# Performance work log

Hardware: AMD Instinct MI355X
Metric: run time of the kernel (lower is better)

## Reference

```python
import jax, jax.numpy as jnp
import numpy as np

B, N3, N4, DIM, HEADS, MLP = 256, 256, 64, 512, 8, 2048
EPS = 1e-5

def _sinusoid(n_position, d_hid):
    pos = np.arange(n_position)[:, None].astype(np.float64)
    i = np.arange(d_hid)[None, :]
    angle = pos / np.power(10000.0, 2 * (i // 2) / d_hid)
    tab = np.empty((n_position, d_hid))
    tab[:, 0::2] = np.sin(angle[:, 0::2])
    tab[:, 1::2] = np.cos(angle[:, 1::2])
    return jnp.asarray(tab[None], dtype=jnp.float32)  # [1, n, d]

def _ln(x, g, b):
    m = x.mean(-1, keepdims=True)
    v = ((x - m) ** 2).mean(-1, keepdims=True)
    return (x - m) / jnp.sqrt(v + EPS) * g + b

def setup_inputs() -> dict:
    key = jax.random.key(0)
    ks = jax.random.split(key, 12)
    s = 0.02
    d = {
        'f3': jax.random.normal(ks[0], (B, N3, DIM), jnp.float32),
        'f4': jax.random.normal(ks[1], (B, N4, DIM), jnp.float32),
        'pos3': _sinusoid(N3, DIM),
        'pos4': _sinusoid(N4, DIM),
        'ln1_g': jnp.ones((DIM,), jnp.float32), 'ln1_b': jnp.zeros((DIM,), jnp.float32),
        'ln2_g': jnp.ones((DIM,), jnp.float32), 'ln2_b': jnp.zeros((DIM,), jnp.float32),
        'ln3_g': jnp.ones((DIM,), jnp.float32), 'ln3_b': jnp.zeros((DIM,), jnp.float32),
        'Wq': jax.random.normal(ks[2], (DIM, DIM), jnp.float32) * s, 'bq': jnp.zeros((DIM,), jnp.float32),
        'Wk': jax.random.normal(ks[3], (DIM, DIM), jnp.float32) * s, 'bk': jnp.zeros((DIM,), jnp.float32),
        'Wv': jax.random.normal(ks[4], (DIM, DIM), jnp.float32) * s, 'bv': jnp.zeros((DIM,), jnp.float32),
        'Wr': jax.random.normal(ks[5], (DIM, DIM), jnp.float32) * s, 'br': jnp.zeros((DIM,), jnp.float32),
        'W1': jax.random.normal(ks[6], (DIM, MLP), jnp.float32) * s, 'b1': jnp.zeros((MLP,), jnp.float32),
        'W2': jax.random.normal(ks[7], (MLP, DIM), jnp.float32) * s, 'b2': jnp.zeros((DIM,), jnp.float32),
    }
    return d

def reference(f3, f4, pos3, pos4, ln1_g, ln1_b, ln2_g, ln2_b, ln3_g, ln3_b,
              Wq, bq, Wk, bk, Wv, bv, Wr, br, W1, b1, W2, b2):
    dk = DIM // HEADS
    f3n = _ln(f3, ln1_g, ln1_b)
    f4n = _ln(f4, ln2_g, ln2_b)
    # projections (dropout=0 -> eval mode)
    q = (f3n + pos3) @ Wq + bq  # [B,N3,D]
    k = (f4n + pos4) @ Wk + bk  # [B,N4,D]
    v = f4n @ Wv + bv           # [B,N4,D]
    # split heads along channel dim (contiguous slices == reshape with head major)
    q = q.reshape(B, N3, HEADS, dk).transpose(0, 2, 3, 1)  # [B,H,dk,N3]
    k = k.reshape(B, N4, HEADS, dk).transpose(0, 2, 3, 1)  # [B,H,dk,N4]
    v = v.reshape(B, N4, HEADS, dk).transpose(0, 2, 3, 1)  # [B,H,dv,N4]
    q = jax.nn.softmax(q, axis=2)  # softmax over head channels
    k = jax.nn.softmax(k, axis=3)  # softmax over key positions
    context = jnp.einsum('bhkn,bhvn->bhkv', k, v)          # [B,H,dk,dv]
    att = jnp.einsum('bhkv,bhkn->bhvn', context, q)        # [B,H,dv,N3]
    att = att.transpose(0, 3, 1, 2).reshape(B, N3, DIM)    # concat heads -> [B,N3,D]
    f3 = f3 + (att @ Wr + br)
    h = _ln(f3, ln3_g, ln3_b)
    h = jax.nn.gelu(h @ W1 + b1, approximate=False) @ W2 + b2
    return f3 + h
```

## Files before the change

### kernel.cpp

```cpp
#include <hip/hip_runtime.h>
#include <hip/hip_bf16.h>

typedef __attribute__((ext_vector_type(8))) short short8v;
typedef __attribute__((ext_vector_type(4))) float f32x4;
typedef __hip_bfloat16 bf16;

#define BDIM 512
#define NHEADS 8
#define DK 64
#define NBATCH 256
#define NN3 256
#define NN4 64
#define NMLP 2048

#define GLOAD_LDS16(g, l)                                                  \
  __builtin_amdgcn_global_load_lds(                                        \
      (const __attribute__((address_space(1))) void*)(g),                  \
      (__attribute__((address_space(3))) void*)(l), 16, 0, 0)

__device__ __forceinline__ float bf2f(short s) {
  union { short u[2]; float f; } cv;
  cv.u[0] = 0; cv.u[1] = s;
  return cv.f;
}
__device__ __forceinline__ short f2bf(float x) {
  bf16 h = __float2bfloat16(x);
  return *reinterpret_cast<short*>(&h);
}

__global__ __launch_bounds__(256) void convert_wt_kernel(
    const float* __restrict__ W, bf16* __restrict__ Wt, int K, int N) {
  int idx = blockIdx.x * 256 + threadIdx.x;
  if (idx >= K * N) return;
  int n = idx / K;
  int k = idx - n * K;
  Wt[idx] = __float2bfloat16(W[(size_t)k * N + n]);
}

__global__ __launch_bounds__(256) void ln_kernel(
    const float* __restrict__ x, const float* __restrict__ g,
    const float* __restrict__ beta, const float* __restrict__ pos, int nmod,
    bf16* __restrict__ out1, bf16* __restrict__ out2, bf16* __restrict__ raw) {
  int w = threadIdx.x >> 6, lane = threadIdx.x & 63;
  int row = blockIdx.x * 4 + w;
  int c0 = lane * 8;
  const float* xr = x + (size_t)row * BDIM + c0;
  float4 v0 = *(const float4*)xr;
  float4 v1 = *(const float4*)(xr + 4);
  float f[8] = {v0.x, v0.y, v0.z, v0.w, v1.x, v1.y, v1.z, v1.w};
  float s = 0.f, sq = 0.f;
#pragma unroll
  for (int i = 0; i < 8; i++) {
    s += f[i];
    sq += f[i] * f[i];
  }
#pragma unroll
  for (int o = 1; o <= 32; o <<= 1) {
    s += __shfl_xor(s, o);
    sq += __shfl_xor(sq, o);
  }
  float mean = s * (1.f / BDIM);
  float var = sq * (1.f / BDIM) - mean * mean;
  float rstd = rsqrtf(var + 1e-5f);
  float4 g0 = *(const float4*)(g + c0);
  float4 g1 = *(const float4*)(g + c0 + 4);
  float4 b0 = *(const float4*)(beta + c0);
  float4 b1 = *(const float4*)(beta + c0 + 4);
  float gg[8] = {g0.x, g0.y, g0.z, g0.w, g1.x, g1.y, g1.z, g1.w};
  float bb[8] = {b0.x, b0.y, b0.z, b0.w, b1.x, b1.y, b1.z, b1.w};
  float pv[8] = {};
  if (pos) {
    int n = row % nmod;
    const float* pr = pos + (size_t)n * BDIM + c0;
    float4 p0 = *(const float4*)pr;
    float4 p1 = *(const float4*)(pr + 4);
    pv[0] = p0.x; pv[1] = p0.y; pv[2] = p0.z; pv[3] = p0.w;
    pv[4] = p1.x; pv[5] = p1.y; pv[6] = p1.z; pv[7] = p1.w;
  }
  short8v o1, o2, rw;
#pragma unroll
  for (int i = 0; i < 8; i++) {
    float nv = (f[i] - mean) * rstd * gg[i] + bb[i];
    o1[i] = f2bf(nv + pv[i]);
    o2[i] = f2bf(nv);
    rw[i] = f2bf(f[i]);
  }
  size_t ob = (size_t)row * BDIM + c0;
  *(short8v*)(out1 + ob) = o1;
  if (out2) *(short8v*)(out2 + ob) = o2;
  if (raw) *(short8v*)(raw + ob) = rw;
}

__global__ __launch_bounds__(256) void lnb_kernel(
    const bf16* __restrict__ x, const float* __restrict__ g,
    const float* __restrict__ beta, bf16* __restrict__ out) {
  int w = threadIdx.x >> 6, lane = threadIdx.x & 63;
  int row = blockIdx.x * 4 + w;
  int c0 = lane * 8;
  short8v v = *(const short8v*)(x + (size_t)row * BDIM + c0);
  float f[8];
  float s = 0.f, sq = 0.f;
#pragma unroll
  for (int i = 0; i < 8; i++) {
    f[i] = bf2f(v[i]);
    s += f[i];
    sq += f[i] * f[i];
  }
#pragma unroll
  for (int o = 1; o <= 32; o <<= 1) {
    s += __shfl_xor(s, o);
    sq += __shfl_xor(sq, o);
  }
  float mean = s * (1.f / BDIM);
  float var = sq * (1.f / BDIM) - mean * mean;
  float rstd = rsqrtf(var + 1e-5f);
  float4 g0 = *(const float4*)(g + c0);
  float4 g1 = *(const float4*)(g + c0 + 4);
  float4 b0 = *(const float4*)(beta + c0);
  float4 b1 = *(const float4*)(beta + c0 + 4);
  float gg[8] = {g0.x, g0.y, g0.z, g0.w, g1.x, g1.y, g1.z, g1.w};
  float bb[8] = {b0.x, b0.y, b0.z, b0.w, b1.x, b1.y, b1.z, b1.w};
  short8v o1;
#pragma unroll
  for (int i = 0; i < 8; i++) o1[i] = f2bf((f[i] - mean) * rstd * gg[i] + bb[i]);
  *(short8v*)(out + (size_t)row * BDIM + c0) = o1;
}

template <int EPI>
__global__ __launch_bounds__(512) void gemm_kernel(
    const bf16* __restrict__ X, const bf16* __restrict__ Wt,
    const float* __restrict__ bias, const void* __restrict__ src, void* outp,
    int K, int ldx, int ldw, int N, int gridX) {
  extern __shared__ bf16 lds[];

  int nwg = gridDim.x;
  int cpx = nwg >> 3;
  int bid = blockIdx.x;
  int nb = (bid & 7) * cpx + (bid >> 3);
  int bx = nb % gridX, by = nb / gridX;
  int row0 = by * 128, col0 = bx * 128;

  int t = threadIdx.x, w = t >> 6, lane = t & 63;
  int wr = w >> 2, wc = w & 3;
  int r16 = lane & 15, kg = lane >> 4;
  int srow = lane >> 3;
  int scol = ((lane & 7) ^ srow) * 8;

  const bf16* gA0 = X + (size_t)(row0 + w * 16 + srow) * ldx + scol;
  const bf16* gB0 = Wt + (size_t)(col0 + w * 16 + srow) * ldw + scol;

  f32x4 acc[4][2] = {};

  auto stage = [&](int kt, int buf) {
    bf16* base = lds + buf * 16384;
    int ke = kt << 6;
#pragma unroll
    for (int j = 0; j < 2; j++) {
      GLOAD_LDS16(gA0 + ke + (size_t)j * 8 * ldx, base + (w * 16 + j * 8) * 64);
      GLOAD_LDS16(gB0 + ke + (size_t)j * 8 * ldw,
                  base + 8192 + (w * 16 + j * 8) * 64);
    }
  };

  auto compute = [&](int buf) {
    const char* base = (const char*)(lds + buf * 16384);
#pragma unroll
    for (int ksub = 0; ksub < 2; ksub++) {
      int cc = (ksub * 64 + kg * 16) ^ ((r16 & 7) << 4);
      short8v a[4], b[2];
#pragma unroll
      for (int m = 0; m < 4; m++)
        a[m] = *(const short8v*)(base + (wr * 64 + m * 16 + r16) * 128 + cc);
#pragma unroll
      for (int n = 0; n < 2; n++)
        b[n] = *(const short8v*)(base + 16384 + (wc * 32 + n * 16 + r16) * 128 + cc);
#pragma unroll
      for (int m = 0; m < 4; m++)
#pragma unroll
        for (int n = 0; n < 2; n++)
          acc[m][n] =
              __builtin_amdgcn_mfma_f32_16x16x32_bf16(a[m], b[n], acc[m][n], 0, 0, 0);
    }
  };

  int NT = K >> 6;
  stage(0, 0);
  stage(1, 1);
  for (int tt = 0; tt < NT; tt++) {
    if (tt < NT - 1)
      asm volatile("s_waitcnt vmcnt(4)" ::: "memory");
    else
      asm volatile("s_waitcnt vmcnt(0)" ::: "memory");
    __builtin_amdgcn_s_barrier();
    asm volatile("" ::: "memory");
    compute(tt & 1);
    asm volatile("" ::: "memory");
    __builtin_amdgcn_s_barrier();
    asm volatile("" ::: "memory");
    if (tt + 2 < NT) stage(tt + 2, tt & 1);
  }

#pragma unroll
  for (int n = 0; n < 2; n++) {
    int col = col0 + wc * 32 + n * 16 + r16;
    float bv = bias ? bias[col] : 0.f;
#pragma unroll
    for (int m = 0; m < 4; m++)
#pragma unroll
      for (int r = 0; r < 4; r++) {
        int row = row0 + wr * 64 + m * 16 + kg * 4 + r;
        size_t o = (size_t)row * N + col;
        float val = acc[m][n][r] + bv;
        if (EPI == 0) {
          ((bf16*)outp)[o] = __float2bfloat16(val);
        } else if (EPI == 1) {
          float gl = 0.5f * val * (1.f + erff(val * 0.70710678f));
          ((bf16*)outp)[o] = __float2bfloat16(gl);
        } else if (EPI == 3) {
          ((bf16*)outp)[o] = __float2bfloat16(bf2f(((const short*)src)[o]) + val);
        } else {
          ((float*)outp)[o] = bf2f(((const short*)src)[o]) + val;
        }
      }
  }
}

__global__ __launch_bounds__(256) void ctx_kernel(
    const bf16* __restrict__ kproj, const bf16* __restrict__ vbuf,
    bf16* __restrict__ ctxT) {
  int bh = blockIdx.x;
  int b = bh >> 3, h = bh & 7;
  __shared__ bf16 lk[NN4][DK], lv[NN4][DK];
  int t = threadIdx.x;
#pragma unroll
  for (int i = 0; i < 16; i++) {
    int idx = i * 256 + t;
    int n = idx >> 6, c = idx & 63;
    size_t gaddr = (size_t)b * NN4 * BDIM + (size_t)n * BDIM + h * DK + c;
    lk[n][c] = kproj[gaddr];
    lv[n][c] = vbuf[gaddr];
  }
  __syncthreads();
  if (t < 64) {
    int c = t;
    float e[NN4];
    float m = -1e30f;
#pragma unroll
    for (int n = 0; n < NN4; n++) {
      e[n] = bf2f(*(short*)&lk[n][c]);
      m = fmaxf(m, e[n]);
    }
    float s = 0.f;
#pragma unroll
    for (int n = 0; n < NN4; n++) {
      e[n] = __expf(e[n] - m);
      s += e[n];
    }
    float inv = 1.f / s;
#pragma unroll
    for (int n = 0; n < NN4; n++) lk[n][c] = __float2bfloat16(e[n] * inv);
  }
  __syncthreads();
  int vc = t >> 2;
  int kc0 = (t & 3) * 16;
  float acc[16] = {};
  for (int n = 0; n < NN4; n++) {
    float vv = __bfloat162float(lv[n][vc]);
#pragma unroll
    for (int i = 0; i < 16; i++)
      acc[i] += vv * __bfloat162float(lk[n][kc0 + i]);
  }
  size_t o = (size_t)bh * 4096 + (size_t)vc * 64 + kc0;
#pragma unroll
  for (int i = 0; i < 16; i++) ctxT[o + i] = __float2bfloat16(acc[i]);
}

__global__ __launch_bounds__(256) void att_kernel(
    const bf16* __restrict__ qproj, const bf16* __restrict__ ctxT,
    bf16* __restrict__ att) {
  int bh = blockIdx.x;
  int b = bh >> 3, h = bh & 7;
  int t = threadIdx.x, w = t >> 6, lane = t & 63;
  int r16 = lane & 15, kg = lane >> 4;
  f32x4 acc[4][4] = {};
  const bf16* qb = qproj + (size_t)b * NN3 * BDIM + h * DK;
  const bf16* cb = ctxT + (size_t)bh * 4096;
  short8v bb[2][4];
#pragma unroll
  for (int kt = 0; kt < 2; kt++)
#pragma unroll
    for (int ni = 0; ni < 4; ni++)
      bb[kt][ni] = *(const short8v*)(cb + (ni * 16 + r16) * 64 + kt * 32 + kg * 8);
#pragma unroll
  for (int mi = 0; mi < 4; mi++) {
    int rrow = w * 64 + mi * 16 + r16;
    short8v a0 = *(const short8v*)(qb + (size_t)rrow * BDIM + kg * 8);
    short8v a1 = *(const short8v*)(qb + (size_t)rrow * BDIM + 32 + kg * 8);
    float f[16];
#pragma unroll
    for (int i = 0; i < 8; i++) {
      f[i] = bf2f(a0[i]);
      f[8 + i] = bf2f(a1[i]);
    }
    float m = f[0];
#pragma unroll
    for (int i = 1; i < 16; i++) m = fmaxf(m, f[i]);
    m = fmaxf(m, __shfl_xor(m, 16));
    m = fmaxf(m, __shfl_xor(m, 32));
    float s = 0.f;
#pragma unroll
    for (int i = 0; i < 16; i++) {
      f[i] = __expf(f[i] - m);
      s += f[i];
    }
    s += __shfl_xor(s, 16);
    s += __shfl_xor(s, 32);
    float inv = 1.f / s;
    short8v A0, A1;
#pragma unroll
    for (int i = 0; i < 8; i++) {
      A0[i] = f2bf(f[i] * inv);
      A1[i] = f2bf(f[8 + i] * inv);
    }
#pragma unroll
    for (int ni = 0; ni < 4; ni++) {
      acc[mi][ni] = __builtin_amdgcn_mfma_f32_16x16x32_bf16(A0, bb[0][ni], acc[mi][ni], 0, 0, 0);
      acc[mi][ni] = __builtin_amdgcn_mfma_f32_16x16x32_bf16(A1, bb[1][ni], acc[mi][ni], 0, 0, 0);
    }
  }
#pragma unroll
  for (int mi = 0; mi < 4; mi++)
#pragma unroll
    for (int ni = 0; ni < 4; ni++)
#pragma unroll
      for (int r = 0; r < 4; r++) {
        int row = w * 64 + mi * 16 + kg * 4 + r;
        int col = ni * 16 + r16;
        att[(size_t)(b * NN3 + row) * BDIM + h * DK + col] =
            __float2bfloat16(acc[mi][ni][r]);
      }
}

extern "C" void kernel_launch(void* const* d_in, const int* in_sizes, int n_in,
                              void* d_out, int out_size, void* d_ws, size_t ws_size,
                              hipStream_t stream) {
  const float* f3 = (const float*)d_in[0];
  const float* f4 = (const float*)d_in[1];
  const float* pos3 = (const float*)d_in[2];
  const float* pos4 = (const float*)d_in[3];
  const float* ln1_g = (const float*)d_in[4];
  const float* ln1_b = (const float*)d_in[5];
  const float* ln2_g = (const float*)d_in[6];
  const float* ln2_b = (const float*)d_in[7];
  const float* ln3_g = (const float*)d_in[8];
  const float* ln3_b = (const float*)d_in[9];
  const float* Wq = (const float*)d_in[10];
  const float* bq = (const float*)d_in[11];
  const float* Wk = (const float*)d_in[12];
  const float* bk = (const float*)d_in[13];
  const float* Wv = (const float*)d_in[14];
  const float* bv = (const float*)d_in[15];
  const float* Wr = (const float*)d_in[16];
  const float* br = (const float*)d_in[17];
  const float* W1 = (const float*)d_in[18];
  const float* b1 = (const float*)d_in[19];
  const float* W2 = (const float*)d_in[20];
  const float* b2 = (const float*)d_in[21];
  float* out = (float*)d_out;

  const int M3 = NBATCH * NN3;
  const int M4 = NBATCH * NN4;
  const int MC = M3 / 2;

  char* ws = (char*)d_ws;
  size_t off = 0;
  auto alloc = [&](size_t bytes) {
    size_t r = off;
    off = (off + bytes + 255) & ~(size_t)255;
    return r;
  };
  size_t oWqt = alloc((size_t)BDIM * BDIM * 2);
  size_t oWkt = alloc((size_t)BDIM * BDIM * 2);
  size_t oWvt = alloc((size_t)BDIM * BDIM * 2);
  size_t oWrt = alloc((size_t)BDIM * BDIM * 2);
  size_t oW1t = alloc((size_t)BDIM * NMLP * 2);
  size_t oW2t = alloc((size_t)BDIM * NMLP * 2);
  size_t oXQ = alloc((size_t)M3 * BDIM * 2);
  size_t oXK = alloc((size_t)M4 * BDIM * 2);
  size_t oXV = alloc((size_t)M4 * BDIM * 2);
  size_t oQF = alloc((size_t)M3 * BDIM * 2);
  size_t oKF = alloc((size_t)M4 * BDIM * 2);
  size_t oVF = alloc((size_t)M4 * BDIM * 2);
  size_t oF3B = alloc((size_t)M3 * BDIM * 2);
  size_t oCT = alloc((size_t)NBATCH * NHEADS * DK * DK * 2);
  size_t oH1 = alloc((size_t)MC * NMLP * 2);
  (void)ws_size;

  bf16* Wqt = (bf16*)(ws + oWqt);
  bf16* Wkt = (bf16*)(ws + oWkt);
  bf16* Wvt = (bf16*)(ws + oWvt);
  bf16* Wrt = (bf16*)(ws + oWrt);
  bf16* W1t = (bf16*)(ws + oW1t);
  bf16* W2t = (bf16*)(ws + oW2t);
  bf16* XQ = (bf16*)(ws + oXQ);
  bf16* XK = (bf16*)(ws + oXK);
  bf16* XV = (bf16*)(ws + oXV);
  bf16* QF = (bf16*)(ws + oQF);
  bf16* KF = (bf16*)(ws + oKF);
  bf16* VF = (bf16*)(ws + oVF);
  bf16* F3B = (bf16*)(ws + oF3B);
  bf16* CT = (bf16*)(ws + oCT);
  bf16* H1 = (bf16*)(ws + oH1);
  bf16* ATT = XQ;
  bf16* F3O = QF;
  bf16* YN = XQ;

  hipFuncSetAttribute((const void*)gemm_kernel<0>,
                      hipFuncAttributeMaxDynamicSharedMemorySize, 65536);
  hipFuncSetAttribute((const void*)gemm_kernel<1>,
                      hipFuncAttributeMaxDynamicSharedMemorySize, 65536);
  hipFuncSetAttribute((const void*)gemm_kernel<3>,
                      hipFuncAttributeMaxDynamicSharedMemorySize, 65536);
  hipFuncSetAttribute((const void*)gemm_kernel<4>,
                      hipFuncAttributeMaxDynamicSharedMemorySize, 65536);

  convert_wt_kernel<<<(BDIM * BDIM + 255) / 256, 256, 0, stream>>>(Wq, Wqt, BDIM, BDIM);
  convert_wt_kernel<<<(BDIM * BDIM + 255) / 256, 256, 0, stream>>>(Wk, Wkt, BDIM, BDIM);
  convert_wt_kernel<<<(BDIM * BDIM + 255) / 256, 256, 0, stream>>>(Wv, Wvt, BDIM, BDIM);
  convert_wt_kernel<<<(BDIM * BDIM + 255) / 256, 256, 0, stream>>>(Wr, Wrt, BDIM, BDIM);
  convert_wt_kernel<<<(BDIM * NMLP + 255) / 256, 256, 0, stream>>>(W1, W1t, BDIM, NMLP);
  convert_wt_kernel<<<(BDIM * NMLP + 255) / 256, 256, 0, stream>>>(W2, W2t, NMLP, BDIM);

  ln_kernel<<<M3 / 4, 256, 0, stream>>>(f3, ln1_g, ln1_b, pos3, NN3, XQ, nullptr, F3B);
  ln_kernel<<<M4 / 4, 256, 0, stream>>>(f4, ln2_g, ln2_b, pos4, NN4, XK, XV, nullptr);

  gemm_kernel<0><<<(BDIM / 128) * (M3 / 128), 512, 65536, stream>>>(
      XQ, Wqt, bq, nullptr, QF, BDIM, BDIM, BDIM, BDIM, BDIM / 128);
  gemm_kernel<0><<<(BDIM / 128) * (M4 / 128), 512, 65536, stream>>>(
      XK, Wkt, bk, nullptr, KF, BDIM, BDIM, BDIM, BDIM, BDIM / 128);
  gemm_kernel<0><<<(BDIM / 128) * (M4 / 128), 512, 65536, stream>>>(
      XV, Wvt, bv, nullptr, VF, BDIM, BDIM, BDIM, BDIM, BDIM / 128);

  ctx_kernel<<<NBATCH * NHEADS, 256, 0, stream>>>(KF, VF, CT);
  att_kernel<<<NBATCH * NHEADS, 256, 0, stream>>>(QF, CT, ATT);

  gemm_kernel<3><<<(BDIM / 128) * (M3 / 128), 512, 65536, stream>>>(
      ATT, Wrt, br, F3B, F3O, BDIM, BDIM, BDIM, BDIM, BDIM / 128);

  lnb_kernel<<<M3 / 4, 256, 0, stream>>>(F3O, ln3_g, ln3_b, YN);

  for (int c = 0; c < 2; c++) {
    const bf16* Yc = YN + (size_t)c * MC * BDIM;
    const bf16* Fc = F3O + (size_t)c * MC * BDIM;
    float* outc = out + (size_t)c * MC * BDIM;
    gemm_kernel<1><<<(NMLP / 128) * (MC / 128), 512, 65536, stream>>>(
        Yc, W1t, b1, nullptr, H1, BDIM, BDIM, BDIM, NMLP, NMLP / 128);
    gemm_kernel<4><<<(BDIM / 128) * (MC / 128), 512, 65536, stream>>>(
        H1, W2t, b2, Fc, outc, NMLP, NMLP, NMLP, BDIM, BDIM / 128);
  }
}
```

Before: 773.1 us.

## Add 256x256-tile GEMM for large projections and tiled weight transpose

Introduces a 256x256 output tile GEMM variant (8 waves, 8x4 MFMA fragments per wave, 128KB LDS double buffer) used for the Q projection, residual projection and both MLP GEMMs, raising arithmetic intensity per LDS load. Also replaces the strided per-element weight transpose-convert kernel with an LDS-tiled 32x32 transpose for coalesced reads and writes. The larger tile uses many more accumulator registers and more LDS, which may limit occupancy and reduces the number of workgroups, so some GEMMs may fill the GPU's compute units less evenly.

```diff
diff --git a/kernel.cpp b/kernel.cpp
--- a/kernel.cpp
+++ b/kernel.cpp
@@ -28,13 +28,18 @@
   return *reinterpret_cast<short*>(&h);
 }
 
-__global__ __launch_bounds__(256) void convert_wt_kernel(
+__global__ __launch_bounds__(256) void convt_kernel(
     const float* __restrict__ W, bf16* __restrict__ Wt, int K, int N) {
-  int idx = blockIdx.x * 256 + threadIdx.x;
-  if (idx >= K * N) return;
-  int n = idx / K;
-  int k = idx - n * K;
-  Wt[idx] = __float2bfloat16(W[(size_t)k * N + n]);
+  __shared__ float tile[32][33];
+  int bx = blockIdx.x * 32, by = blockIdx.y * 32;
+  int tx = threadIdx.x, ty = threadIdx.y;
+#pragma unroll
+  for (int j = 0; j < 32; j += 8)
+    tile[ty + j][tx] = W[(size_t)(by + ty + j) * N + bx + tx];
+  __syncthreads();
+#pragma unroll
+  for (int j = 0; j < 32; j += 8)
+    Wt[(size_t)(bx + ty + j) * K + by + tx] = __float2bfloat16(tile[tx][ty + j]);
 }
 
 __global__ __launch_bounds__(256) void ln_kernel(
@@ -209,6 +214,105 @@
 #pragma unroll
       for (int r = 0; r < 4; r++) {
         int row = row0 + wr * 64 + m * 16 + kg * 4 + r;
+        size_t o = (size_t)row * N + col;
+        float val = acc[m][n][r] + bv;
+        if (EPI == 0) {
+          ((bf16*)outp)[o] = __float2bfloat16(val);
+        } else if (EPI == 1) {
+          float gl = 0.5f * val * (1.f + erff(val * 0.70710678f));
+          ((bf16*)outp)[o] = __float2bfloat16(gl);
+        } else if (EPI == 3) {
+          ((bf16*)outp)[o] = __float2bfloat16(bf2f(((const short*)src)[o]) + val);
+        } else {
+          ((float*)outp)[o] = bf2f(((const short*)src)[o]) + val;
+        }
+      }
+  }
+}
+
+template <int EPI>
+__global__ __launch_bounds__(512, 2) void gemm256_kernel(
+    const bf16* __restrict__ X, const bf16* __restrict__ Wt,
+    const float* __restrict__ bias, const void* __restrict__ src, void* outp,
+    int K, int ldx, int ldw, int N, int gridX) {
+  extern __shared__ bf16 lds[];
+
+  int nwg = gridDim.x;
+  int cpx = nwg >> 3;
+  int bid = blockIdx.x;
+  int nb = (bid & 7) * cpx + (bid >> 3);
+  int bx = nb % gridX, by = nb / gridX;
+  int row0 = by * 256, col0 = bx * 256;
+
+  int t = threadIdx.x, w = t >> 6, lane = t & 63;
+  int wr = w >> 2, wc = w & 3;
+  int r16 = lane & 15, kg = lane >> 4;
+  int srow = lane >> 3;
+  int scol = ((lane & 7) ^ srow) * 8;
+
+  const bf16* gA0 = X + (size_t)(row0 + w * 32 + srow) * ldx + scol;
+  const bf16* gB0 = Wt + (size_t)(col0 + w * 32 + srow) * ldw + scol;
+
+  f32x4 acc[8][4] = {};
+
+  auto stage = [&](int kt, int buf) {
+    bf16* base = lds + buf * 32768;
+    int ke = kt << 6;
+#pragma unroll
+    for (int j = 0; j < 4; j++) {
+      GLOAD_LDS16(gA0 + ke + (size_t)j * 8 * ldx, base + (w * 32 + j * 8) * 64);
+      GLOAD_LDS16(gB0 + ke + (size_t)j * 8 * ldw,
+                  base + 16384 + (w * 32 + j * 8) * 64);
+    }
+  };
+
+  auto compute = [&](int buf) {
+    const char* base = (const char*)(lds + buf * 32768);
+#pragma unroll
+    for (int ksub = 0; ksub < 2; ksub++) {
+      int cc = (ksub * 64 + kg * 16) ^ ((r16 & 7) << 4);
+      short8v a[8], b[4];
+#pragma unroll
+      for (int m = 0; m < 8; m++)
+        a[m] = *(const short8v*)(base + (wr * 128 + m * 16 + r16) * 128 + cc);
+#pragma unroll
+      for (int n = 0; n < 4; n++)
+        b[n] = *(const short8v*)(base + 32768 + (wc * 64 + n * 16 + r16) * 128 + cc);
+#pragma unroll
+      for (int m = 0; m < 8; m++)
+#pragma unroll
+        for (int n = 0; n < 4; n++)
+          acc[m][n] =
+              __builtin_amdgcn_mfma_f32_16x16x32_bf16(a[m], b[n], acc[m][n], 0, 0, 0);
+    }
+  };
+
+  int NT = K >> 6;
+  stage(0, 0);
+  stage(1, 1);
+  for (int tt = 0; tt < NT; tt++) {
+    if (tt < NT - 1)
+      asm volatile("s_waitcnt vmcnt(8)" ::: "memory");
+    else
+      asm volatile("s_waitcnt vmcnt(0)" ::: "memory");
+    __builtin_amdgcn_s_barrier();
+    asm volatile("" ::: "memory");
+    compute(tt & 1);
+    asm volatile("" ::: "memory");
+    __builtin_amdgcn_s_barrier();
+    asm volatile("" ::: "memory");
+    if (tt + 2 < NT) stage(tt + 2, tt & 1);
+  }
+
+#pragma unroll
+  for (int n = 0; n < 4; n++) {
+    int col = col0 + wc * 64 + n * 16 + r16;
+    float bv = bias ? bias[col] : 0.f;
+#pragma unroll
+    for (int m = 0; m < 8; m++)
+#pragma unroll
+      for (int r = 0; r < 4; r++) {
+        int row = row0 + wr * 128 + m * 16 + kg * 4 + r;
         size_t o = (size_t)row * N + col;
         float val = acc[m][n][r] + bv;
         if (EPI == 0) {
@@ -417,25 +521,27 @@
 
   hipFuncSetAttribute((const void*)gemm_kernel<0>,
                       hipFuncAttributeMaxDynamicSharedMemorySize, 65536);
-  hipFuncSetAttribute((const void*)gemm_kernel<1>,
-                      hipFuncAttributeMaxDynamicSharedMemorySize, 65536);
-  hipFuncSetAttribute((const void*)gemm_kernel<3>,
-                      hipFuncAttributeMaxDynamicSharedMemorySize, 65536);
-  hipFuncSetAttribute((const void*)gemm_kernel<4>,
-                      hipFuncAttributeMaxDynamicSharedMemorySize, 65536);
-
-  convert_wt_kernel<<<(BDIM * BDIM + 255) / 256, 256, 0, stream>>>(Wq, Wqt, BDIM, BDIM);
-  convert_wt_kernel<<<(BDIM * BDIM + 255) / 256, 256, 0, stream>>>(Wk, Wkt, BDIM, BDIM);
-  convert_wt_kernel<<<(BDIM * BDIM + 255) / 256, 256, 0, stream>>>(Wv, Wvt, BDIM, BDIM);
-  convert_wt_kernel<<<(BDIM * BDIM + 255) / 256, 256, 0, stream>>>(Wr, Wrt, BDIM, BDIM);
-  convert_wt_kernel<<<(BDIM * NMLP + 255) / 256, 256, 0, stream>>>(W1, W1t, BDIM, NMLP);
-  convert_wt_kernel<<<(BDIM * NMLP + 255) / 256, 256, 0, stream>>>(W2, W2t, NMLP, BDIM);
+  hipFuncSetAttribute((const void*)gemm256_kernel<0>,
+                      hipFuncAttributeMaxDynamicSharedMemorySize, 131072);
+  hipFuncSetAttribute((const void*)gemm256_kernel<1>,
+                      hipFuncAttributeMaxDynamicSharedMemorySize, 131072);
+  hipFuncSetAttribute((const void*)gemm256_kernel<3>,
+                      hipFuncAttributeMaxDynamicSharedMemorySize, 131072);
+  hipFuncSetAttribute((const void*)gemm256_kernel<4>,
+                      hipFuncAttributeMaxDynamicSharedMemorySize, 131072);
+
+  convt_kernel<<<dim3(BDIM / 32, BDIM / 32), dim3(32, 8), 0, stream>>>(Wq, Wqt, BDIM, BDIM);
+  convt_kernel<<<dim3(BDIM / 32, BDIM / 32), dim3(32, 8), 0, stream>>>(Wk, Wkt, BDIM, BDIM);
+  convt_kernel<<<dim3(BDIM / 32, BDIM / 32), dim3(32, 8), 0, stream>>>(Wv, Wvt, BDIM, BDIM);
+  convt_kernel<<<dim3(BDIM / 32, BDIM / 32), dim3(32, 8), 0, stream>>>(Wr, Wrt, BDIM, BDIM);
+  convt_kernel<<<dim3(NMLP / 32, BDIM / 32), dim3(32, 8), 0, stream>>>(W1, W1t, BDIM, NMLP);
+  convt_kernel<<<dim3(BDIM / 32, NMLP / 32), dim3(32, 8), 0, stream>>>(W2, W2t, NMLP, BDIM);
 
   ln_kernel<<<M3 / 4, 256, 0, stream>>>(f3, ln1_g, ln1_b, pos3, NN3, XQ, nullptr, F3B);
   ln_kernel<<<M4 / 4, 256, 0, stream>>>(f4, ln2_g, ln2_b, pos4, NN4, XK, XV, nullptr);
 
-  gemm_kernel<0><<<(BDIM / 128) * (M3 / 128), 512, 65536, stream>>>(
-      XQ, Wqt, bq, nullptr, QF, BDIM, BDIM, BDIM, BDIM, BDIM / 128);
+  gemm256_kernel<0><<<(BDIM / 256) * (M3 / 256), 512, 131072, stream>>>(
+      XQ, Wqt, bq, nullptr, QF, BDIM, BDIM, BDIM, BDIM, BDIM / 256);
   gemm_kernel<0><<<(BDIM / 128) * (M4 / 128), 512, 65536, stream>>>(
       XK, Wkt, bk, nullptr, KF, BDIM, BDIM, BDIM, BDIM, BDIM / 128);
   gemm_kernel<0><<<(BDIM / 128) * (M4 / 128), 512, 65536, stream>>>(
@@ -444,8 +550,8 @@
   ctx_kernel<<<NBATCH * NHEADS, 256, 0, stream>>>(KF, VF, CT);
   att_kernel<<<NBATCH * NHEADS, 256, 0, stream>>>(QF, CT, ATT);
 
-  gemm_kernel<3><<<(BDIM / 128) * (M3 / 128), 512, 65536, stream>>>(
-      ATT, Wrt, br, F3B, F3O, BDIM, BDIM, BDIM, BDIM, BDIM / 128);
+  gemm256_kernel<3><<<(BDIM / 256) * (M3 / 256), 512, 131072, stream>>>(
+      ATT, Wrt, br, F3B, F3O, BDIM, BDIM, BDIM, BDIM, BDIM / 256);
 
   lnb_kernel<<<M3 / 4, 256, 0, stream>>>(F3O, ln3_g, ln3_b, YN);
 
@@ -453,9 +559,9 @@
     const bf16* Yc = YN + (size_t)c * MC * BDIM;
     const bf16* Fc = F3O + (size_t)c * MC * BDIM;
     float* outc = out + (size_t)c * MC * BDIM;
-    gemm_kernel<1><<<(NMLP / 128) * (MC / 128), 512, 65536, stream>>>(
-        Yc, W1t, b1, nullptr, H1, BDIM, BDIM, BDIM, NMLP, NMLP / 128);
-    gemm_kernel<4><<<(BDIM / 128) * (MC / 128), 512, 65536, stream>>>(
-        H1, W2t, b2, Fc, outc, NMLP, NMLP, NMLP, BDIM, BDIM / 128);
-  }
-}
+    gemm256_kernel<1><<<(NMLP / 256) * (MC / 256), 512, 131072, stream>>>(
+        Yc, W1t, b1, nullptr, H1, BDIM, BDIM, BDIM, NMLP, NMLP / 256);
+    gemm256_kernel<4><<<(BDIM / 256) * (MC / 256), 512, 131072, stream>>>(
+        H1, W2t, b2, Fc, outc, NMLP, NMLP, NMLP, BDIM, BDIM / 256);
+  }
+}
```

Result: slower. 926.1 us (+19.8%).
